# Performance work log

Measured on AMD Instinct MI355X. Metric: run time of the kernel, lower is better.

The kernel has to match this reference:

```python
import jax, jax.numpy as jnp
import numpy as np

B, C, L = 8, 256, 2048        # batch, query_dim, seq len
HEADS, DIM_HEAD = 4, 32
HIDDEN = HEADS * DIM_HEAD      # 128
EPS = 1e-05
SCALE = DIM_HEAD ** -0.5


def setup_inputs() -> dict:
    key = jax.random.key(0)
    ks = jax.random.split(key, 8)
    s_in = 1.0 / np.sqrt(C)
    s_h = 1.0 / np.sqrt(HIDDEN)
    return {
        "x": jax.random.normal(ks[0], (B, C, L), dtype=jnp.float32),
        "g": jnp.ones((1, C, 1), dtype=jnp.float32),
        "b": jnp.zeros((1, C, 1), dtype=jnp.float32),
        "Wq": jax.random.normal(ks[1], (HIDDEN, C), dtype=jnp.float32) * s_in,
        "Wk": jax.random.normal(ks[2], (HIDDEN, C), dtype=jnp.float32) * s_in,
        "Wv": jax.random.normal(ks[3], (HIDDEN, C), dtype=jnp.float32) * s_in,
        "Wo": jax.random.normal(ks[4], (C, HIDDEN), dtype=jnp.float32) * s_h,
        "bo": jnp.zeros((C,), dtype=jnp.float32),
    }


def reference(x, g, b, Wq, Wk, Wv, Wo, bo):
    og_x = x
    # channel-dim LayerNorm (dim=1), biased variance
    mean = jnp.mean(x, axis=1, keepdims=True)
    var = jnp.var(x, axis=1, keepdims=True)
    xn = (x - mean) / jnp.sqrt(var + EPS) * g + b          # [B, C, L]
    xt = jnp.transpose(xn, (0, 2, 1))                      # [B, L, C]
    # QKV projections (self-attention: context = normed x)
    q = xt @ Wq.T                                          # [B, L, HIDDEN]
    k = xt @ Wk.T
    v = xt @ Wv.T
    # b (h c) d layout: [B, HEADS, DIM_HEAD, L]
    split = lambda t: jnp.transpose(t, (0, 2, 1)).reshape(B, HEADS, DIM_HEAD, L)
    q, k, v = split(q), split(k), split(v)
    # scores over head-channel dim c -> [B, H, L, L]
    qk = jnp.einsum('bhcd,bhce->bhde', q, k) * SCALE
    attn = jax.nn.softmax(qk, axis=-1)
    out = jnp.einsum('bhde,bhce->bhcd', attn, v)           # [B, H, DIM_HEAD, L]
    out = out.reshape(B, HIDDEN, L)
    # 1x1 Conv1d: hidden -> query_dim
    y = jnp.einsum('oc,bcl->bol', Wo, out) + bo[None, :, None]
    return y + og_x
```

## Files before the change

kernel.cpp:

```cpp
#include <hip/hip_runtime.h>
#include <math.h>

#define BB_ 8
#define CC_ 256
#define LL_ 2048
#define HEADS_ 4
#define DHEAD_ 32
#define HID_ 128
#define EPS_ 1e-5f
#define SCALE_ 0.17677669529663687f
#define K1_ (SCALE_ * 1.44269504088896f)

typedef short v8s  __attribute__((ext_vector_type(8)));
typedef float v4f  __attribute__((ext_vector_type(4)));
typedef float v16f __attribute__((ext_vector_type(16)));
typedef unsigned v4u __attribute__((ext_vector_type(4)));

__device__ inline short f2bf(float x) {
    union { float f; unsigned u; } a; a.f = x;
    unsigned r = a.u + 0x7fffu + ((a.u >> 16) & 1u);
    return (short)(r >> 16);
}
__device__ inline unsigned fbits(float x) { union { float f; unsigned u; } a; a.f = x; return a.u; }

__global__ __launch_bounds__(256) void k_prep(
    const float* __restrict__ Wq, const float* __restrict__ Wk, const float* __restrict__ Wv,
    const float* __restrict__ Wo, short* __restrict__ wqkv, short* __restrict__ wo)
{
    int idx = blockIdx.x * 256 + threadIdx.x;
    if (idx < 384 * 256) {
        int o = idx >> 8, c = idx & 255;
        float s;
        if (o < 128)      s = Wq[o * 256 + c];
        else if (o < 256) s = Wk[(o - 128) * 256 + c];
        else              s = Wv[(o - 256) * 256 + c];
        wqkv[idx] = f2bf(s);
    } else {
        int i2 = idx - 384 * 256;
        wo[i2] = f2bf(Wo[i2]);
    }
}

__global__ __launch_bounds__(512) void k_ln_qkv(
    const float* __restrict__ x, const float* __restrict__ g, const float* __restrict__ bvec,
    const short* __restrict__ wqkv,
    short* __restrict__ q, short* __restrict__ k, short* __restrict__ v)
{
    __shared__ float xn[CC_ * 33];
    __shared__ short xnT[32 * 264];
    __shared__ short st2[128 * 48];
    __shared__ float ps_[16 * 32], ps2_[16 * 32];
    __shared__ float cmean[32], crstd[32];
    const int b   = blockIdx.y;
    const int l0  = blockIdx.x * 32;
    const int tid = threadIdx.x;

    for (int idx = tid; idx < CC_ * 32; idx += 512) {
        int c = idx >> 5, ls = idx & 31;
        xn[c * 33 + ls] = x[((size_t)b * CC_ + c) * LL_ + l0 + ls];
    }
    __syncthreads();

    {
        int part = tid >> 5, col = tid & 31;
        float s = 0.f, s2 = 0.f;
        #pragma unroll
        for (int cc = 0; cc < 16; ++cc) {
            float t = xn[(part * 16 + cc) * 33 + col];
            s += t; s2 += t * t;
        }
        ps_[part * 32 + col] = s; ps2_[part * 32 + col] = s2;
    }
    __syncthreads();
    if (tid < 32) {
        float s = 0.f, s2 = 0.f;
        #pragma unroll
        for (int p = 0; p < 16; ++p) { s += ps_[p * 32 + tid]; s2 += ps2_[p * 32 + tid]; }
        float mean = s * (1.f / CC_);
        float var  = s2 * (1.f / CC_) - mean * mean;
        cmean[tid] = mean;
        crstd[tid] = rsqrtf(var + EPS_);
    }
    __syncthreads();

    for (int idx = tid; idx < 32 * 128; idx += 512) {
        int ls = idx >> 7, cc = idx & 127;
        int c0 = 2 * cc, c1 = 2 * cc + 1;
        float mu = cmean[ls], rs = crstd[ls];
        float a0 = (xn[c0 * 33 + ls] - mu) * rs * g[c0] + bvec[c0];
        float a1 = (xn[c1 * 33 + ls] - mu) * rs * g[c1] + bvec[c1];
        xnT[ls * 264 + c0]     = f2bf(a0);
        xnT[ls * 264 + c0 + 1] = f2bf(a1);
    }
    __syncthreads();

    const int wave = tid >> 6, lane = tid & 63;
    const int n = lane & 15, quad = lane >> 4;
    const int rowbase = (wave >> 2) * 16;
    const int colbase = (wave & 3) * 96;

    v4f acc[6];
    #pragma unroll
    for (int ct = 0; ct < 6; ++ct) acc[ct] = (v4f){0.f, 0.f, 0.f, 0.f};

    #pragma unroll
    for (int ks = 0; ks < 8; ++ks) {
        const v8s af = *(const v8s*)(xnT + (rowbase + n) * 264 + ks * 32 + quad * 8);
        #pragma unroll
        for (int ct = 0; ct < 6; ++ct) {
            const v8s bfrag = *(const v8s*)(wqkv + (size_t)(colbase + ct * 16 + n) * 256 + ks * 32 + quad * 8);
            acc[ct] = __builtin_amdgcn_mfma_f32_16x16x32_bf16(af, bfrag, acc[ct], 0, 0, 0);
        }
    }
    __syncthreads();

    #pragma unroll
    for (int ct = 0; ct < 6; ++ct) {
        int o = colbase + ct * 16 + n;
        #pragma unroll
        for (int r = 0; r < 4; ++r) {
            int l = rowbase + quad * 4 + r;
            float val = acc[ct][r];
            if (o < 128)      xnT[l * 264 + o] = f2bf(val * K1_);
            else if (o < 256) xnT[l * 264 + o] = f2bf(val);
            else              st2[(o - 256) * 48 + l] = f2bf(val);
        }
    }
    __syncthreads();

    {
        int u = tid;
        int h = u >> 7, rest = u & 127;
        int l = rest >> 2, dg = rest & 3;
        size_t bh = (size_t)b * HEADS_ + h;
        v8s qv = *(const v8s*)(xnT + l * 264 + h * 32 + dg * 8);
        *(v8s*)(q + (bh * LL_ + l0 + l) * DHEAD_ + dg * 8) = qv;
        v8s kv = *(const v8s*)(xnT + l * 264 + 128 + h * 32 + dg * 8);
        *(v8s*)(k + (bh * LL_ + l0 + l) * DHEAD_ + dg * 8) = kv;

        int op = u >> 2, lg = u & 3;
        v8s vv = *(const v8s*)(st2 + op * 48 + lg * 8);
        int h2 = op >> 5, d = op & 31;
        *(v8s*)(v + (((size_t)b * HEADS_ + h2) * DHEAD_ + d) * LL_ + l0 + lg * 8) = vv;
    }
}

__global__ __launch_bounds__(512) void k_attn(
    const short* __restrict__ q, const short* __restrict__ k, const short* __restrict__ v,
    short* __restrict__ ao)
{
    __shared__ float Ost[4][32][32];
    __shared__ float psumst[4 * 32];
    const int bh   = blockIdx.y;
    const int b    = bh >> 2, h = bh & 3;
    const int tid  = threadIdx.x;
    const int wave = tid >> 6, lane = tid & 63;
    const int wq   = wave & 3;
    const int kh   = wave >> 2;
    const int m    = lane & 31;
    const int half = lane >> 5;
    const size_t kvbase = (size_t)bh * LL_ * DHEAD_;
    const size_t vbase  = (size_t)bh * DHEAD_ * LL_;

    const int q0 = blockIdx.x * 128 + wq * 32;
    const int kb = kh * 1024;

    const v8s qf0 = *(const v8s*)(q + kvbase + (size_t)(q0 + m) * DHEAD_ + half * 8);
    const v8s qf1 = *(const v8s*)(q + kvbase + (size_t)(q0 + m) * DHEAD_ + 16 + half * 8);

    v16f O = {};
    float psum = 0.f;

    v8s kf0 = *(const v8s*)(k + kvbase + (size_t)(kb + m) * DHEAD_ + half * 8);
    v8s kf1 = *(const v8s*)(k + kvbase + (size_t)(kb + m) * DHEAD_ + 16 + half * 8);
    v8s vf0 = *(const v8s*)(v + vbase + (size_t)m * LL_ + kb + half * 8);
    v8s vf1 = *(const v8s*)(v + vbase + (size_t)m * LL_ + kb + 16 + half * 8);

    for (int kt = 0; kt < 1024; kt += 32) {
        v16f S = __builtin_amdgcn_mfma_f32_32x32x16_bf16(kf0, qf0, (v16f){}, 0, 0, 0);
        S      = __builtin_amdgcn_mfma_f32_32x32x16_bf16(kf1, qf1, S,        0, 0, 0);

        const int ktn = kb + ((kt + 32) & 1023);
        kf0 = *(const v8s*)(k + kvbase + (size_t)(ktn + m) * DHEAD_ + half * 8);
        kf1 = *(const v8s*)(k + kvbase + (size_t)(ktn + m) * DHEAD_ + 16 + half * 8);
        v8s vf0n = *(const v8s*)(v + vbase + (size_t)m * LL_ + ktn + half * 8);
        v8s vf1n = *(const v8s*)(v + vbase + (size_t)m * LL_ + ktn + 16 + half * 8);

        unsigned e[8];
        #pragma unroll
        for (int i = 0; i < 8; ++i) {
            float pa = __builtin_amdgcn_exp2f(S[2 * i]);
            float pb = __builtin_amdgcn_exp2f(S[2 * i + 1]);
            psum += pa + pb;
            e[i] = __builtin_amdgcn_perm(fbits(pb) + 0x8000u, fbits(pa) + 0x8000u, 0x07060302u);
        }
        v4u f1, f2;
#if __has_builtin(__builtin_amdgcn_permlane32_swap)
        {
            auto r02 = __builtin_amdgcn_permlane32_swap(e[0], e[2], false, false);
            auto r13 = __builtin_amdgcn_permlane32_swap(e[1], e[3], false, false);
            auto r46 = __builtin_amdgcn_permlane32_swap(e[4], e[6], false, false);
            auto r57 = __builtin_amdgcn_permlane32_swap(e[5], e[7], false, false);
            f1 = (v4u){r02[0], r13[0], r02[1], r13[1]};
            f2 = (v4u){r46[0], r57[0], r46[1], r57[1]};
        }
#else
        {
            unsigned o0 = __shfl_xor(e[0], 32, 64), o1 = __shfl_xor(e[1], 32, 64);
            unsigned o2 = __shfl_xor(e[2], 32, 64), o3 = __shfl_xor(e[3], 32, 64);
            unsigned o4 = __shfl_xor(e[4], 32, 64), o5 = __shfl_xor(e[5], 32, 64);
            unsigned o6 = __shfl_xor(e[6], 32, 64), o7 = __shfl_xor(e[7], 32, 64);
            f1 = half ? (v4u){o2, o3, e[2], e[3]} : (v4u){e[0], e[1], o0, o1};
            f2 = half ? (v4u){o6, o7, e[6], e[7]} : (v4u){e[4], e[5], o4, o5};
        }
#endif
        O = __builtin_amdgcn_mfma_f32_32x32x16_bf16(__builtin_bit_cast(v8s, f1), vf0, O, 0, 0, 0);
        O = __builtin_amdgcn_mfma_f32_32x32x16_bf16(__builtin_bit_cast(v8s, f2), vf1, O, 0, 0, 0);

        vf0 = vf0n; vf1 = vf1n;
    }

    psum += __shfl_xor(psum, 32, 64);

    if (kh == 1) {
        #pragma unroll
        for (int r = 0; r < 16; ++r) {
            int qr = (r & 3) + 8 * (r >> 2) + 4 * half;
            Ost[wq][qr][m] = O[r];
        }
        if (half == 0) psumst[wq * 32 + m] = psum;
    }
    __syncthreads();
    if (kh == 0) {
        float den = psum + psumst[wq * 32 + m];
        float invden = 1.f / den;
        #pragma unroll
        for (int r = 0; r < 16; ++r) {
            int qr = (r & 3) + 8 * (r >> 2) + 4 * half;
            float inv = __shfl(invden, qr, 64);
            float val = (O[r] + Ost[wq][qr][m]) * inv;
            int row = q0 + qr;
            ao[((size_t)b * LL_ + row) * HID_ + h * DHEAD_ + m] = f2bf(val);
        }
    }
}

__global__ __launch_bounds__(256) void k_oproj(
    const short* __restrict__ ao, const short* __restrict__ wo, const float* __restrict__ bo,
    const float* __restrict__ x, float* __restrict__ out)
{
    const int b = blockIdx.y;
    const int l0 = blockIdx.x * 16;
    const int tid = threadIdx.x;
    const int wave = tid >> 6, lane = tid & 63;
    const int n = lane & 15, quad = lane >> 4;

    v8s bf[4];
    #pragma unroll
    for (int ks = 0; ks < 4; ++ks)
        bf[ks] = *(const v8s*)(ao + ((size_t)b * LL_ + l0 + n) * HID_ + ks * 32 + quad * 8);

    #pragma unroll
    for (int oi_ = 0; oi_ < 4; ++oi_) {
        int ot = wave * 4 + oi_;
        v4f acc = {0.f, 0.f, 0.f, 0.f};
        #pragma unroll
        for (int ks = 0; ks < 4; ++ks) {
            const v8s af = *(const v8s*)(wo + (size_t)(ot * 16 + n) * HID_ + ks * 32 + quad * 8);
            acc = __builtin_amdgcn_mfma_f32_16x16x32_bf16(af, bf[ks], acc, 0, 0, 0);
        }
        #pragma unroll
        for (int r = 0; r < 4; ++r) {
            int o = ot * 16 + quad * 4 + r;
            size_t oi = ((size_t)b * CC_ + o) * LL_ + l0 + n;
            out[oi] = acc[r] + bo[o] + x[oi];
        }
    }
}

extern "C" void kernel_launch(void* const* d_in, const int* in_sizes, int n_in,
                              void* d_out, int out_size, void* d_ws, size_t ws_size,
                              hipStream_t stream) {
    const float* x  = (const float*)d_in[0];
    const float* g  = (const float*)d_in[1];
    const float* bv = (const float*)d_in[2];
    const float* Wq = (const float*)d_in[3];
    const float* Wk = (const float*)d_in[4];
    const float* Wv = (const float*)d_in[5];
    const float* Wo = (const float*)d_in[6];
    const float* bo = (const float*)d_in[7];
    float* out = (float*)d_out;

    const size_t qkv_elems = (size_t)BB_ * HEADS_ * LL_ * DHEAD_;
    short* q    = (short*)d_ws;
    short* k    = q + qkv_elems;
    short* v    = k + qkv_elems;
    short* ao   = v + qkv_elems;
    short* wqkv = ao + qkv_elems;
    short* wo   = wqkv + 384 * 256;

    k_prep  <<<dim3((384 * 256 + 256 * 128) / 256), dim3(256), 0, stream>>>(Wq, Wk, Wv, Wo, wqkv, wo);
    k_ln_qkv<<<dim3(LL_ / 32, BB_), dim3(512), 0, stream>>>(x, g, bv, wqkv, q, k, v);
    k_attn  <<<dim3(LL_ / 128, BB_ * HEADS_), dim3(512), 0, stream>>>(q, k, v, ao);
    k_oproj <<<dim3(LL_ / 16, BB_), dim3(256), 0, stream>>>(ao, wo, bo, x, out);
}
```

Before: 174.5 us.

## Fold LayerNorm affine into QKV weights, software-pipeline QK MFMA, split oproj grid

The LayerNorm gamma, beta and the softmax scale are folded into the bf16 QKV weights. The weight-prep kernel also precomputes per-output sums, so the QKV kernel projects raw x and applies mean and rstd as an epilogue correction. The LN statistics pass is fused with the global load, which removes one barrier and the elementwise normalize step. The attention loop computes the next tile's QK scores one iteration ahead so MFMA overlaps the exp and permute work, and the output projection grid is doubled along output channels for more parallelism. Projecting un-normalized x in bf16 and then subtracting mean*sum(w*g) risks cancellation and lower accuracy.

```diff
diff --git a/kernel.cpp b/kernel.cpp
--- a/kernel.cpp
+++ b/kernel.cpp
@@ -25,76 +25,80 @@
 
 __global__ __launch_bounds__(256) void k_prep(
     const float* __restrict__ Wq, const float* __restrict__ Wk, const float* __restrict__ Wv,
-    const float* __restrict__ Wo, short* __restrict__ wqkv, short* __restrict__ wo)
+    const float* __restrict__ Wo, const float* __restrict__ g, const float* __restrict__ bvec,
+    short* __restrict__ wqkv, short* __restrict__ wo, float2* __restrict__ gb)
 {
-    int idx = blockIdx.x * 256 + threadIdx.x;
-    if (idx < 384 * 256) {
-        int o = idx >> 8, c = idx & 255;
-        float s;
-        if (o < 128)      s = Wq[o * 256 + c];
-        else if (o < 256) s = Wk[(o - 128) * 256 + c];
-        else              s = Wv[(o - 256) * 256 + c];
-        wqkv[idx] = f2bf(s);
+    __shared__ float red0[256], red1[256];
+    const int blk = blockIdx.x, c = threadIdx.x;
+    if (blk < 384) {
+        const float* W; int oo; float scale = 1.f;
+        if (blk < 128)      { W = Wq; oo = blk;       scale = K1_; }
+        else if (blk < 256) { W = Wk; oo = blk - 128; }
+        else                { W = Wv; oo = blk - 256; }
+        float w  = W[oo * 256 + c] * scale;
+        float wg = w * g[c];
+        wqkv[blk * 256 + c] = f2bf(wg);
+        red0[c] = wg;
+        red1[c] = w * bvec[c];
+        __syncthreads();
+        for (int s = 128; s > 0; s >>= 1) {
+            if (c < s) { red0[c] += red0[c + s]; red1[c] += red1[c + s]; }
+            __syncthreads();
+        }
+        if (c == 0) gb[blk] = make_float2(red0[0], red1[0]);
     } else {
-        int i2 = idx - 384 * 256;
+        int i2 = (blk - 384) * 256 + c;
         wo[i2] = f2bf(Wo[i2]);
     }
 }
 
 __global__ __launch_bounds__(512) void k_ln_qkv(
-    const float* __restrict__ x, const float* __restrict__ g, const float* __restrict__ bvec,
-    const short* __restrict__ wqkv,
+    const float* __restrict__ x, const short* __restrict__ wqkv, const float2* __restrict__ gb,
     short* __restrict__ q, short* __restrict__ k, short* __restrict__ v)
 {
     __shared__ float xn[CC_ * 33];
     __shared__ short xnT[32 * 264];
     __shared__ short st2[128 * 48];
-    __shared__ float ps_[16 * 32], ps2_[16 * 32];
-    __shared__ float cmean[32], crstd[32];
+    __shared__ float ps_[8 * 32], ps2_[8 * 32];
+    __shared__ float rs_s[32], rsmu_s[32];
     const int b   = blockIdx.y;
     const int l0  = blockIdx.x * 32;
     const int tid = threadIdx.x;
-
-    for (int idx = tid; idx < CC_ * 32; idx += 512) {
-        int c = idx >> 5, ls = idx & 31;
-        xn[c * 33 + ls] = x[((size_t)b * CC_ + c) * LL_ + l0 + ls];
-    }
-    __syncthreads();
+    const int wave = tid >> 6, lane = tid & 63;
 
     {
-        int part = tid >> 5, col = tid & 31;
+        const int ls = tid & 31;
         float s = 0.f, s2 = 0.f;
         #pragma unroll
-        for (int cc = 0; cc < 16; ++cc) {
-            float t = xn[(part * 16 + cc) * 33 + col];
+        for (int kk = 0; kk < 16; ++kk) {
+            int c = (tid >> 5) + 16 * kk;
+            float t = x[((size_t)b * CC_ + c) * LL_ + l0 + ls];
+            xn[c * 33 + ls] = t;
             s += t; s2 += t * t;
         }
-        ps_[part * 32 + col] = s; ps2_[part * 32 + col] = s2;
+        s  += __shfl_xor(s, 32, 64);
+        s2 += __shfl_xor(s2, 32, 64);
+        if (lane < 32) { ps_[wave * 32 + lane] = s; ps2_[wave * 32 + lane] = s2; }
     }
     __syncthreads();
     if (tid < 32) {
         float s = 0.f, s2 = 0.f;
         #pragma unroll
-        for (int p = 0; p < 16; ++p) { s += ps_[p * 32 + tid]; s2 += ps2_[p * 32 + tid]; }
+        for (int p = 0; p < 8; ++p) { s += ps_[p * 32 + tid]; s2 += ps2_[p * 32 + tid]; }
         float mean = s * (1.f / CC_);
         float var  = s2 * (1.f / CC_) - mean * mean;
-        cmean[tid] = mean;
-        crstd[tid] = rsqrtf(var + EPS_);
-    }
-    __syncthreads();
-
+        float rs   = rsqrtf(var + EPS_);
+        rs_s[tid]   = rs;
+        rsmu_s[tid] = rs * mean;
+    }
     for (int idx = tid; idx < 32 * 128; idx += 512) {
         int ls = idx >> 7, cc = idx & 127;
-        int c0 = 2 * cc, c1 = 2 * cc + 1;
-        float mu = cmean[ls], rs = crstd[ls];
-        float a0 = (xn[c0 * 33 + ls] - mu) * rs * g[c0] + bvec[c0];
-        float a1 = (xn[c1 * 33 + ls] - mu) * rs * g[c1] + bvec[c1];
-        xnT[ls * 264 + c0]     = f2bf(a0);
-        xnT[ls * 264 + c0 + 1] = f2bf(a1);
-    }
-    __syncthreads();
-
-    const int wave = tid >> 6, lane = tid & 63;
+        int c0 = 2 * cc;
+        xnT[ls * 264 + c0]     = f2bf(xn[c0 * 33 + ls]);
+        xnT[ls * 264 + c0 + 1] = f2bf(xn[(c0 + 1) * 33 + ls]);
+    }
+    __syncthreads();
+
     const int n = lane & 15, quad = lane >> 4;
     const int rowbase = (wave >> 2) * 16;
     const int colbase = (wave & 3) * 96;
@@ -114,15 +118,21 @@
     }
     __syncthreads();
 
+    float rsv[4], rmv[4];
+    #pragma unroll
+    for (int r = 0; r < 4; ++r) {
+        int l = rowbase + quad * 4 + r;
+        rsv[r] = rs_s[l]; rmv[r] = rsmu_s[l];
+    }
     #pragma unroll
     for (int ct = 0; ct < 6; ++ct) {
         int o = colbase + ct * 16 + n;
+        float2 gbo = gb[o];
         #pragma unroll
         for (int r = 0; r < 4; ++r) {
             int l = rowbase + quad * 4 + r;
-            float val = acc[ct][r];
-            if (o < 128)      xnT[l * 264 + o] = f2bf(val * K1_);
-            else if (o < 256) xnT[l * 264 + o] = f2bf(val);
+            float val = rsv[r] * acc[ct][r] - rmv[r] * gbo.x + gbo.y;
+            if (o < 256)      xnT[l * 264 + o] = f2bf(val);
             else              st2[(o - 256) * 48 + l] = f2bf(val);
         }
     }
@@ -171,20 +181,25 @@
     v16f O = {};
     float psum = 0.f;
 
-    v8s kf0 = *(const v8s*)(k + kvbase + (size_t)(kb + m) * DHEAD_ + half * 8);
-    v8s kf1 = *(const v8s*)(k + kvbase + (size_t)(kb + m) * DHEAD_ + 16 + half * 8);
-    v8s vf0 = *(const v8s*)(v + vbase + (size_t)m * LL_ + kb + half * 8);
-    v8s vf1 = *(const v8s*)(v + vbase + (size_t)m * LL_ + kb + 16 + half * 8);
+    #define LDK_(pos, off) (*(const v8s*)(k + kvbase + (size_t)((pos) + m) * DHEAD_ + (off) + half * 8))
+    #define LDV_(pos, off) (*(const v8s*)(v + vbase + (size_t)m * LL_ + (pos) + (off) + half * 8))
+
+    v8s vf0 = LDV_(kb, 0), vf1 = LDV_(kb, 16);
+    v8s kn0 = LDK_(kb + 32, 0), kn1 = LDK_(kb + 32, 16);
+    v16f S;
+    {
+        v8s kf0 = LDK_(kb, 0), kf1 = LDK_(kb, 16);
+        S = __builtin_amdgcn_mfma_f32_32x32x16_bf16(kf0, qf0, (v16f){}, 0, 0, 0);
+        S = __builtin_amdgcn_mfma_f32_32x32x16_bf16(kf1, qf1, S,        0, 0, 0);
+    }
 
     for (int kt = 0; kt < 1024; kt += 32) {
-        v16f S = __builtin_amdgcn_mfma_f32_32x32x16_bf16(kf0, qf0, (v16f){}, 0, 0, 0);
-        S      = __builtin_amdgcn_mfma_f32_32x32x16_bf16(kf1, qf1, S,        0, 0, 0);
-
         const int ktn = kb + ((kt + 32) & 1023);
-        kf0 = *(const v8s*)(k + kvbase + (size_t)(ktn + m) * DHEAD_ + half * 8);
-        kf1 = *(const v8s*)(k + kvbase + (size_t)(ktn + m) * DHEAD_ + 16 + half * 8);
-        v8s vf0n = *(const v8s*)(v + vbase + (size_t)m * LL_ + ktn + half * 8);
-        v8s vf1n = *(const v8s*)(v + vbase + (size_t)m * LL_ + ktn + 16 + half * 8);
+        const int kt2 = kb + ((kt + 64) & 1023);
+        v16f Sn = __builtin_amdgcn_mfma_f32_32x32x16_bf16(kn0, qf0, (v16f){}, 0, 0, 0);
+        Sn      = __builtin_amdgcn_mfma_f32_32x32x16_bf16(kn1, qf1, Sn,        0, 0, 0);
+        kn0 = LDK_(kt2, 0); kn1 = LDK_(kt2, 16);
+        v8s vn0 = LDV_(ktn, 0), vn1 = LDV_(ktn, 16);
 
         unsigned e[8];
         #pragma unroll
@@ -217,8 +232,10 @@
         O = __builtin_amdgcn_mfma_f32_32x32x16_bf16(__builtin_bit_cast(v8s, f1), vf0, O, 0, 0, 0);
         O = __builtin_amdgcn_mfma_f32_32x32x16_bf16(__builtin_bit_cast(v8s, f2), vf1, O, 0, 0, 0);
 
-        vf0 = vf0n; vf1 = vf1n;
-    }
+        S = Sn; vf0 = vn0; vf1 = vn1;
+    }
+    #undef LDK_
+    #undef LDV_
 
     psum += __shfl_xor(psum, 32, 64);
 
@@ -249,8 +266,9 @@
     const short* __restrict__ ao, const short* __restrict__ wo, const float* __restrict__ bo,
     const float* __restrict__ x, float* __restrict__ out)
 {
-    const int b = blockIdx.y;
+    const int b = blockIdx.z;
     const int l0 = blockIdx.x * 16;
+    const int obase = blockIdx.y * 8;
     const int tid = threadIdx.x;
     const int wave = tid >> 6, lane = tid & 63;
     const int n = lane & 15, quad = lane >> 4;
@@ -261,8 +279,8 @@
         bf[ks] = *(const v8s*)(ao + ((size_t)b * LL_ + l0 + n) * HID_ + ks * 32 + quad * 8);
 
     #pragma unroll
-    for (int oi_ = 0; oi_ < 4; ++oi_) {
-        int ot = wave * 4 + oi_;
+    for (int oi_ = 0; oi_ < 2; ++oi_) {
+        int ot = obase + wave * 2 + oi_;
         v4f acc = {0.f, 0.f, 0.f, 0.f};
         #pragma unroll
         for (int ks = 0; ks < 4; ++ks) {
@@ -298,9 +316,10 @@
     short* ao   = v + qkv_elems;
     short* wqkv = ao + qkv_elems;
     short* wo   = wqkv + 384 * 256;
-
-    k_prep  <<<dim3((384 * 256 + 256 * 128) / 256), dim3(256), 0, stream>>>(Wq, Wk, Wv, Wo, wqkv, wo);
-    k_ln_qkv<<<dim3(LL_ / 32, BB_), dim3(512), 0, stream>>>(x, g, bv, wqkv, q, k, v);
+    float2* gb  = (float2*)(wo + 256 * 128);
+
+    k_prep  <<<dim3(512), dim3(256), 0, stream>>>(Wq, Wk, Wv, Wo, g, bv, wqkv, wo, gb);
+    k_ln_qkv<<<dim3(LL_ / 32, BB_), dim3(512), 0, stream>>>(x, wqkv, gb, q, k, v);
     k_attn  <<<dim3(LL_ / 128, BB_ * HEADS_), dim3(512), 0, stream>>>(q, k, v, ao);
-    k_oproj <<<dim3(LL_ / 16, BB_), dim3(256), 0, stream>>>(ao, wo, bo, x, out);
-}
+    k_oproj <<<dim3(LL_ / 16, 2, BB_), dim3(256), 0, stream>>>(ao, wo, bo, x, out);
+}
```

Result: no change. 173.6 us (-0.6%).
